# Optimization experiments

Measured on AMD Instinct MI355X. Metric: run time of the kernel, lower is better.

## Reference

```python
import jax, jax.numpy as jnp
import numpy as np

N_NODES = 50000
N_EDGES = 600000
D_IN = 128
HID = 128
N_SAGE = 2          # num_layers - 1
N_GRAPHS = 512
BN_EPS = 1e-5


def setup_inputs() -> dict:
    key = jax.random.key(0)
    ks = jax.random.split(key, 12)
    s = 1.0 / np.sqrt(HID)
    x = jax.random.normal(ks[0], (N_NODES, D_IN), dtype=jnp.float32)
    edge_index = jax.random.randint(ks[1], (2, N_EDGES), 0, N_NODES, dtype=jnp.int32)
    batch = jnp.sort(jax.random.randint(ks[2], (N_NODES,), 0, N_GRAPHS, dtype=jnp.int32))
    # GIN MLP: Linear(D_IN,HID) -> ReLU -> Linear(HID,HID)
    gin_w1 = jax.random.normal(ks[3], (D_IN, HID), dtype=jnp.float32) * s
    gin_b1 = jnp.zeros((HID,), jnp.float32)
    gin_w2 = jax.random.normal(ks[4], (HID, HID), dtype=jnp.float32) * s
    gin_b2 = jnp.zeros((HID,), jnp.float32)
    # SAGEConv layers: lin_l (neighbors, with bias), lin_r (root, no bias)
    sage_wl = jax.random.normal(ks[5], (N_SAGE, HID, HID), dtype=jnp.float32) * s
    sage_bl = jnp.zeros((N_SAGE, HID), jnp.float32)
    sage_wr = jax.random.normal(ks[6], (N_SAGE, HID, HID), dtype=jnp.float32) * s
    # BatchNorm per layer (3 layers)
    bn_gamma = jnp.ones((1 + N_SAGE, HID), jnp.float32)
    bn_beta = jnp.zeros((1 + N_SAGE, HID), jnp.float32)
    return {"x": x, "edge_index": edge_index, "batch": batch,
            "gin_w1": gin_w1, "gin_b1": gin_b1, "gin_w2": gin_w2, "gin_b2": gin_b2,
            "sage_wl": sage_wl, "sage_bl": sage_bl, "sage_wr": sage_wr,
            "bn_gamma": bn_gamma, "bn_beta": bn_beta}


def _batchnorm(h, gamma, beta):
    # training-mode BN over the node dimension (biased variance, as torch)
    mu = jnp.mean(h, axis=0)
    var = jnp.var(h, axis=0)
    return gamma * (h - mu) * jax.lax.rsqrt(var + BN_EPS) + beta


def reference(x, edge_index, batch, gin_w1, gin_b1, gin_w2, gin_b2,
              sage_wl, sage_bl, sage_wr, bn_gamma, bn_beta):
    n = x.shape[0]
    src, dst = edge_index[0], edge_index[1]

    # ---- Layer 0: GINConv (eps=0): mlp(x + sum_{j->i} x_j) ----
    agg = jax.ops.segment_sum(x[src], dst, num_segments=n)  # [N, D_IN]
    h = x + agg
    h = jax.nn.relu(h @ gin_w1 + gin_b1) @ gin_w2 + gin_b2
    h = jax.nn.relu(_batchnorm(h, bn_gamma[0], bn_beta[0]))
    # dropout is identity (eval mode)

    # degree for mean aggregation (shared across SAGE layers)
    deg = jax.ops.segment_sum(jnp.ones((src.shape[0],), h.dtype), dst, num_segments=n)
    inv_deg = (1.0 / jnp.maximum(deg, 1.0))[:, None]  # [N,1]

    # ---- SAGE layers: lin_l(mean_{j->i} h_j) + lin_r(h_i) ----
    for l in range(N_SAGE):
        neigh = jax.ops.segment_sum(h[src], dst, num_segments=n) * inv_deg
        h = neigh @ sage_wl[l] + sage_bl[l] + h @ sage_wr[l]
        h = jax.nn.relu(_batchnorm(h, bn_gamma[l + 1], bn_beta[l + 1]))

    # ---- global mean pool over batch ids ----
    sums = jax.ops.segment_sum(h, batch, num_segments=N_GRAPHS)  # [G, HID]
    counts = jax.ops.segment_sum(jnp.ones((n,), h.dtype), batch, num_segments=N_GRAPHS)
    return sums / jnp.maximum(counts, 1.0)[:, None]
```

## Files before the change

### kernel.cpp

```cpp
#include <hip/hip_runtime.h>

#define N_NODES 50000
#define N_EDGES 600000
#define HID 128
#define N_GRAPHS 512
#define BN_EPS 1e-5f
#define INV_N (1.0f / 50000.0f)

typedef __attribute__((ext_vector_type(8))) short bf16x8;
typedef __attribute__((ext_vector_type(4))) float f32x4;

__device__ __forceinline__ unsigned short f2b(float f) {
    unsigned u = __float_as_uint(f);
    return (unsigned short)((u + 0x7FFFu + ((u >> 16) & 1u)) >> 16);
}
__device__ __forceinline__ float b2f(unsigned short h) {
    return __uint_as_float(((unsigned)h) << 16);
}

#define CONVX_BLOCKS 6250
#define WCONV_BLOCKS 384
#define DEG_BLOCKS   2344
__global__ __launch_bounds__(256) void prep_kernel(
    const float* __restrict__ x, const float* __restrict__ gw1, const float* __restrict__ gw2,
    const float* __restrict__ swl, const float* __restrict__ swr, const int* __restrict__ dst,
    unsigned short* __restrict__ x16, unsigned short* __restrict__ wt, int* __restrict__ deg)
{
    int b = blockIdx.x;
    int t = threadIdx.x;
    if (b < CONVX_BLOCKS) {
        int gid = b * 256 + t;
        int i = gid >> 5, l = gid & 31;
        if (i >= N_NODES) return;
        int c0 = l * 4;
        float4 v = *(const float4*)(x + (size_t)i * 128 + c0);
        ushort4 o;
        o.x = f2b(v.x); o.y = f2b(v.y); o.z = f2b(v.z); o.w = f2b(v.w);
        *(ushort4*)(x16 + (size_t)i * 128 + c0) = o;
    } else if (b < CONVX_BLOCKS + WCONV_BLOCKS) {
        int gid = (b - CONVX_BLOCKS) * 256 + t;
        int m = gid >> 14;
        int e = gid & 16383;
        int k = e >> 7;
        int n = e & 127;
        const float* src = (m == 0) ? gw1 : (m == 1) ? gw2 : (m == 2) ? swl
                         : (m == 3) ? swr : (m == 4) ? (swl + 16384) : (swr + 16384);
        wt[m * 16384 + n * 128 + k] = f2b(src[k * 128 + n]);
    } else {
        int e = (b - CONVX_BLOCKS - WCONV_BLOCKS) * 256 + t;
        if (e < N_EDGES) atomicAdd(&deg[dst[e]], 1);
    }
}

#define ALLOC_BLOCKS 196
__global__ __launch_bounds__(256) void alloc_kernel(int* __restrict__ cursor,
                                                    int* __restrict__ row_beg,
                                                    float* __restrict__ inv_deg,
                                                    int* __restrict__ total,
                                                    const int* __restrict__ batch,
                                                    int* __restrict__ gstart) {
    if (blockIdx.x >= ALLOC_BLOCKS) {
        int g = (blockIdx.x - ALLOC_BLOCKS) * 256 + threadIdx.x;
        if (g > N_GRAPHS) return;
        int lo = 0, hi = N_NODES;
        while (lo < hi) {
            int mid = (lo + hi) >> 1;
            if (batch[mid] < g) lo = mid + 1; else hi = mid;
        }
        gstart[g] = lo;
        return;
    }
    __shared__ int tmp[256];
    __shared__ int base;
    int i = blockIdx.x * 256 + threadIdx.x;
    int d = (i < N_NODES) ? cursor[i] : 0;
    tmp[threadIdx.x] = d;
    __syncthreads();
#pragma unroll
    for (int off = 1; off < 256; off <<= 1) {
        int v = (threadIdx.x >= off) ? tmp[threadIdx.x - off] : 0;
        __syncthreads();
        tmp[threadIdx.x] += v;
        __syncthreads();
    }
    if (threadIdx.x == 255) base = atomicAdd(total, tmp[255]);
    __syncthreads();
    if (i < N_NODES) {
        int b = base + tmp[threadIdx.x] - d;
        row_beg[i] = b;
        cursor[i] = b;
        inv_deg[i] = 1.0f / fmaxf((float)d, 1.0f);
    }
}

__global__ void csr_fill_kernel(const int* __restrict__ src, const int* __restrict__ dst,
                                int* __restrict__ cursor, int* __restrict__ csr_src, int nE) {
    int e = blockIdx.x * blockDim.x + threadIdx.x;
    if (e < nE) {
        int pos = atomicAdd(&cursor[dst[e]], 1);
        csr_src[pos] = src[e];
    }
}

template<bool AFF, bool MEAN, bool HACT>
__global__ __launch_bounds__(256) void aggregate_kernel(
    const unsigned short* __restrict__ feat,
    const int* __restrict__ row_beg, const int* __restrict__ row_end,
    const int* __restrict__ csr_src,
    const float* __restrict__ stats, const float* __restrict__ gamma,
    const float* __restrict__ beta, const float* __restrict__ inv_deg,
    unsigned short* __restrict__ agg, unsigned short* __restrict__ hact, int n)
{
    int gid = blockIdx.x * blockDim.x + threadIdx.x;
    int node = gid >> 4;
    int lane = gid & 15;
    if (node >= n) return;
    int c0 = lane * 8;

    float cc[8], ss[8];
    if (AFF) {
#pragma unroll
        for (int j = 0; j < 8; j++) {
            int col = c0 + j;
            float mu = stats[col] * INV_N;
            float var = stats[128 + col] * INV_N - mu * mu;
            float rs = rsqrtf(var + BN_EPS);
            float c = gamma[col] * rs;
            cc[j] = c;
            ss[j] = beta[col] - mu * c;
        }
    }

    float a[8];
#pragma unroll
    for (int j = 0; j < 8; j++) a[j] = 0.f;

    int beg = row_beg[node];
    int end = row_end[node];
    int e = beg;
    for (; e + 3 < end; e += 4) {
        int s0 = csr_src[e];
        int s1 = csr_src[e + 1];
        int s2 = csr_src[e + 2];
        int s3 = csr_src[e + 3];
        bf16x8 v0 = *(const bf16x8*)(feat + (size_t)s0 * 128 + c0);
        bf16x8 v1 = *(const bf16x8*)(feat + (size_t)s1 * 128 + c0);
        bf16x8 v2 = *(const bf16x8*)(feat + (size_t)s2 * 128 + c0);
        bf16x8 v3 = *(const bf16x8*)(feat + (size_t)s3 * 128 + c0);
#pragma unroll
        for (int j = 0; j < 8; j++) {
            float t0 = b2f((unsigned short)v0[j]);
            float t1 = b2f((unsigned short)v1[j]);
            float t2 = b2f((unsigned short)v2[j]);
            float t3 = b2f((unsigned short)v3[j]);
            if (AFF) {
                t0 = fmaxf(t0 * cc[j] + ss[j], 0.f);
                t1 = fmaxf(t1 * cc[j] + ss[j], 0.f);
                t2 = fmaxf(t2 * cc[j] + ss[j], 0.f);
                t3 = fmaxf(t3 * cc[j] + ss[j], 0.f);
            }
            a[j] += (t0 + t1) + (t2 + t3);
        }
    }
    for (; e < end; e++) {
        int s0 = csr_src[e];
        bf16x8 v0 = *(const bf16x8*)(feat + (size_t)s0 * 128 + c0);
#pragma unroll
        for (int j = 0; j < 8; j++) {
            float t0 = b2f((unsigned short)v0[j]);
            if (AFF) t0 = fmaxf(t0 * cc[j] + ss[j], 0.f);
            a[j] += t0;
        }
    }

    if (MEAN) {
        float s = inv_deg[node];
#pragma unroll
        for (int j = 0; j < 8; j++) a[j] *= s;
    }
    bf16x8 o;
#pragma unroll
    for (int j = 0; j < 8; j++) o[j] = (short)f2b(a[j]);
    *(bf16x8*)(agg + (size_t)node * 128 + c0) = o;

    if (HACT) {
        bf16x8 v = *(const bf16x8*)(feat + (size_t)node * 128 + c0);
        bf16x8 h;
#pragma unroll
        for (int j = 0; j < 8; j++)
            h[j] = (short)f2b(fmaxf(b2f((unsigned short)v[j]) * cc[j] + ss[j], 0.f));
        *(bf16x8*)(hact + (size_t)node * 128 + c0) = h;
    }
}

__global__ __launch_bounds__(256, 2) void gemm_gin_kernel(
    const unsigned short* __restrict__ X, const unsigned short* __restrict__ AGG,
    const unsigned short* __restrict__ W1t, const unsigned short* __restrict__ W2t,
    const float* __restrict__ b1, const float* __restrict__ b2,
    float* __restrict__ stats, unsigned short* __restrict__ Cb,
    int M, int ntiles)
{
    __shared__ unsigned short t1[32][136];
    __shared__ float red[2][128];

    const int t = threadIdx.x;
    const int wave = t >> 6;
    const int lane = t & 63;
    const int colhalf = wave & 1;
    const int rowpair = wave >> 1;
    const int m16 = lane & 15;
    const int quad = lane >> 4;
    const int k0 = quad * 8;
    const int colbase = colhalf * 64;
    const int lrow = rowpair * 16 + m16;

    const bf16x8 zero8 = {0, 0, 0, 0, 0, 0, 0, 0};

    bf16x8 w1f[4][4], w2f[4][4];
#pragma unroll
    for (int ct = 0; ct < 4; ct++) {
        int col = colbase + ct * 16 + m16;
#pragma unroll
        for (int kc = 0; kc < 4; kc++) {
            w1f[ct][kc] = *(const bf16x8*)(W1t + (size_t)col * 128 + kc * 32 + k0);
            w2f[ct][kc] = *(const bf16x8*)(W2t + (size_t)col * 128 + kc * 32 + k0);
        }
    }
    f32x4 bs1[4], bs2[4];
#pragma unroll
    for (int ct = 0; ct < 4; ct++) {
        bs1[ct] = *(const f32x4*)(b1 + colbase + ct * 16 + quad * 4);
        bs2[ct] = *(const f32x4*)(b2 + colbase + ct * 16 + quad * 4);
    }

    float psum[4][4], psq[4][4];
#pragma unroll
    for (int ct = 0; ct < 4; ct++)
#pragma unroll
        for (int r = 0; r < 4; r++) { psum[ct][r] = 0.f; psq[ct][r] = 0.f; }

    for (int tile = blockIdx.x; tile < ntiles; tile += gridDim.x) {
        int arow = tile * 32 + rowpair * 16 + m16;
        bool aok = arow < M;

        bf16x8 a[4];
#pragma unroll
        for (int kc = 0; kc < 4; kc++) {
            if (aok) {
                bf16x8 vx = *(const bf16x8*)(X + (size_t)arow * 128 + kc * 32 + k0);
                bf16x8 vg = *(const bf16x8*)(AGG + (size_t)arow * 128 + kc * 32 + k0);
                bf16x8 r;
#pragma unroll
                for (int i = 0; i < 8; i++)
                    r[i] = (short)f2b(b2f((unsigned short)vx[i]) + b2f((unsigned short)vg[i]));
                a[kc] = r;
            } else {
                a[kc] = zero8;
            }
        }

        f32x4 acc[4];
#pragma unroll
        for (int ct = 0; ct < 4; ct++) acc[ct] = (f32x4){0.f, 0.f, 0.f, 0.f};
#pragma unroll
        for (int kc = 0; kc < 4; kc++)
#pragma unroll
            for (int ct = 0; ct < 4; ct++)
                acc[ct] = __builtin_amdgcn_mfma_f32_16x16x32_bf16(w1f[ct][kc], a[kc], acc[ct], 0, 0, 0);

        __syncthreads();
#pragma unroll
        for (int ct = 0; ct < 4; ct++) {
            f32x4 v = acc[ct] + bs1[ct];
            ushort4 o;
            o.x = f2b(fmaxf(v[0], 0.f));
            o.y = f2b(fmaxf(v[1], 0.f));
            o.z = f2b(fmaxf(v[2], 0.f));
            o.w = f2b(fmaxf(v[3], 0.f));
            *(ushort4*)&t1[lrow][colbase + ct * 16 + quad * 4] = o;
        }
        __syncthreads();

        bf16x8 ta[4];
#pragma unroll
        for (int kc = 0; kc < 4; kc++)
            ta[kc] = *(const bf16x8*)&t1[lrow][kc * 32 + k0];

        f32x4 acc2[4];
#pragma unroll
        for (int ct = 0; ct < 4; ct++) acc2[ct] = (f32x4){0.f, 0.f, 0.f, 0.f};
#pragma unroll
        for (int kc = 0; kc < 4; kc++)
#pragma unroll
            for (int ct = 0; ct < 4; ct++)
                acc2[ct] = __builtin_amdgcn_mfma_f32_16x16x32_bf16(w2f[ct][kc], ta[kc], acc2[ct], 0, 0, 0);

        int orow = arow;
        if (orow < M) {
#pragma unroll
            for (int ct = 0; ct < 4; ct++) {
                f32x4 v = acc2[ct] + bs2[ct];
                int col = colbase + ct * 16 + quad * 4;
#pragma unroll
                for (int r = 0; r < 4; r++) { psum[ct][r] += v[r]; psq[ct][r] += v[r] * v[r]; }
                ushort4 o;
                o.x = f2b(v[0]); o.y = f2b(v[1]); o.z = f2b(v[2]); o.w = f2b(v[3]);
                *(ushort4*)(Cb + (size_t)orow * 128 + col) = o;
            }
        }
    }

#pragma unroll
    for (int ct = 0; ct < 4; ct++)
#pragma unroll
        for (int r = 0; r < 4; r++) {
#pragma unroll
            for (int mask = 1; mask <= 8; mask <<= 1) {
                psum[ct][r] += __shfl_xor(psum[ct][r], mask, 64);
                psq[ct][r]  += __shfl_xor(psq[ct][r], mask, 64);
            }
        }
    __syncthreads();
    if (m16 == 0) {
#pragma unroll
        for (int ct = 0; ct < 4; ct++)
#pragma unroll
            for (int r = 0; r < 4; r++)
                red[rowpair][colbase + ct * 16 + quad * 4 + r] = psum[ct][r];
    }
    __syncthreads();
    if (t < 128) atomicAdd(&stats[t], red[0][t] + red[1][t]);
    __syncthreads();
    if (m16 == 0) {
#pragma unroll
        for (int ct = 0; ct < 4; ct++)
#pragma unroll
            for (int r = 0; r < 4; r++)
                red[rowpair][colbase + ct * 16 + quad * 4 + r] = psq[ct][r];
    }
    __syncthreads();
    if (t < 128) atomicAdd(&stats[128 + t], red[0][t] + red[1][t]);
}

__global__ __launch_bounds__(256) void gemm_dual_kernel(
    const unsigned short* __restrict__ A1, const unsigned short* __restrict__ A2,
    const unsigned short* __restrict__ W1t, const unsigned short* __restrict__ W2t,
    const float* __restrict__ bias, float* __restrict__ stats,
    unsigned short* __restrict__ Cb, int M, int ntiles)
{
    __shared__ float red[128];

    const int t = threadIdx.x;
    const int wave = t >> 6;
    const int lane = t & 63;
    const int m16 = lane & 15;
    const int quad = lane >> 4;
    const int k0 = quad * 8;
    const int colbase = wave * 32;

    const bf16x8 zero8 = {0, 0, 0, 0, 0, 0, 0, 0};

    bf16x8 w1f[2][4], w2f[2][4];
#pragma unroll
    for (int ct = 0; ct < 2; ct++) {
        int col = colbase + ct * 16 + m16;
#pragma unroll
        for (int kc = 0; kc < 4; kc++) {
            w1f[ct][kc] = *(const bf16x8*)(W1t + (size_t)col * 128 + kc * 32 + k0);
            w2f[ct][kc] = *(const bf16x8*)(W2t + (size_t)col * 128 + kc * 32 + k0);
        }
    }
    f32x4 bs[2];
#pragma unroll
    for (int ct = 0; ct < 2; ct++)
        bs[ct] = *(const f32x4*)(bias + colbase + ct * 16 + quad * 4);

    float psum[2][4], psq[2][4];
#pragma unroll
    for (int ct = 0; ct < 2; ct++)
#pragma unroll
        for (int r = 0; r < 4; r++) { psum[ct][r] = 0.f; psq[ct][r] = 0.f; }

    bf16x8 a1[4], a2[4], a1n[4], a2n[4];

    int tile = blockIdx.x;
    if (tile < ntiles) {
        int arow = tile * 16 + m16;
        bool aok = arow < M;
#pragma unroll
        for (int kc = 0; kc < 4; kc++) {
            a1[kc] = aok ? *(const bf16x8*)(A1 + (size_t)arow * 128 + kc * 32 + k0) : zero8;
            a2[kc] = aok ? *(const bf16x8*)(A2 + (size_t)arow * 128 + kc * 32 + k0) : zero8;
        }
    }

    for (; tile < ntiles; tile += gridDim.x) {
        int nt = tile + gridDim.x;
        if (nt < ntiles) {
            int arow = nt * 16 + m16;
            bool aok = arow < M;
#pragma unroll
            for (int kc = 0; kc < 4; kc++) {
                a1n[kc] = aok ? *(const bf16x8*)(A1 + (size_t)arow * 128 + kc * 32 + k0) : zero8;
                a2n[kc] = aok ? *(const bf16x8*)(A2 + (size_t)arow * 128 + kc * 32 + k0) : zero8;
            }
        }

        f32x4 acc[2];
        acc[0] = (f32x4){0.f, 0.f, 0.f, 0.f};
        acc[1] = (f32x4){0.f, 0.f, 0.f, 0.f};
#pragma unroll
        for (int kc = 0; kc < 4; kc++) {
#pragma unroll
            for (int ct = 0; ct < 2; ct++) {
                acc[ct] = __builtin_amdgcn_mfma_f32_16x16x32_bf16(w1f[ct][kc], a1[kc], acc[ct], 0, 0, 0);
                acc[ct] = __builtin_amdgcn_mfma_f32_16x16x32_bf16(w2f[ct][kc], a2[kc], acc[ct], 0, 0, 0);
            }
        }

        int orow = tile * 16 + m16;
        if (orow < M) {
#pragma unroll
            for (int ct = 0; ct < 2; ct++) {
                f32x4 v = acc[ct] + bs[ct];
                int col = colbase + ct * 16 + quad * 4;
#pragma unroll
                for (int r = 0; r < 4; r++) { psum[ct][r] += v[r]; psq[ct][r] += v[r] * v[r]; }
                ushort4 o;
                o.x = f2b(v[0]); o.y = f2b(v[1]); o.z = f2b(v[2]); o.w = f2b(v[3]);
                *(ushort4*)(Cb + (size_t)orow * 128 + col) = o;
            }
        }

        if (nt < ntiles) {
            a1[0] = a1n[0]; a1[1] = a1n[1]; a1[2] = a1n[2]; a1[3] = a1n[3];
            a2[0] = a2n[0]; a2[1] = a2n[1]; a2[2] = a2n[2]; a2[3] = a2n[3];
        }
    }

#pragma unroll
    for (int ct = 0; ct < 2; ct++)
#pragma unroll
        for (int r = 0; r < 4; r++) {
#pragma unroll
            for (int mask = 1; mask <= 8; mask <<= 1) {
                psum[ct][r] += __shfl_xor(psum[ct][r], mask, 64);
                psq[ct][r]  += __shfl_xor(psq[ct][r], mask, 64);
            }
        }
    if (m16 == 0) {
#pragma unroll
        for (int ct = 0; ct < 2; ct++)
#pragma unroll
            for (int r = 0; r < 4; r++)
                red[colbase + ct * 16 + quad * 4 + r] = psum[ct][r];
    }
    __syncthreads();
    if (t < 128) atomicAdd(&stats[t], red[t]);
    __syncthreads();
    if (m16 == 0) {
#pragma unroll
        for (int ct = 0; ct < 2; ct++)
#pragma unroll
            for (int r = 0; r < 4; r++)
                red[colbase + ct * 16 + quad * 4 + r] = psq[ct][r];
    }
    __syncthreads();
    if (t < 128) atomicAdd(&stats[128 + t], red[t]);
}

__global__ __launch_bounds__(128) void pool_mean_kernel(const unsigned short* __restrict__ h,
                                                        const int* __restrict__ gstart,
                                                        const float* __restrict__ stats,
                                                        const float* __restrict__ gamma,
                                                        const float* __restrict__ beta,
                                                        float* __restrict__ out) {
    int g = blockIdx.x;
    int col = threadIdx.x;
    float mu = stats[col] * INV_N;
    float var = stats[128 + col] * INV_N - mu * mu;
    float rs = rsqrtf(var + BN_EPS);
    float c = gamma[col] * rs;
    float b = beta[col] - mu * c;
    int beg = gstart[g];
    int end = gstart[g + 1];
    float s = 0.f;
    int i = beg;
    for (; i + 1 < end; i += 2) {
        float v0 = b2f(h[(size_t)i * 128 + col]);
        float v1 = b2f(h[(size_t)(i + 1) * 128 + col]);
        s += fmaxf(v0 * c + b, 0.f) + fmaxf(v1 * c + b, 0.f);
    }
    if (i < end)
        s += fmaxf(b2f(h[(size_t)i * 128 + col]) * c + b, 0.f);
    float cnt = fmaxf((float)(end - beg), 1.0f);
    out[(size_t)g * 128 + col] = s / cnt;
}

extern "C" void kernel_launch(void* const* d_in, const int* in_sizes, int n_in,
                              void* d_out, int out_size, void* d_ws, size_t ws_size,
                              hipStream_t stream) {
    const float* x    = (const float*)d_in[0];
    const int*   ei   = (const int*)d_in[1];
    const int*   src  = ei;
    const int*   dst  = ei + N_EDGES;
    const int*   batch = (const int*)d_in[2];
    const float* gw1  = (const float*)d_in[3];
    const float* gb1  = (const float*)d_in[4];
    const float* gw2  = (const float*)d_in[5];
    const float* gb2  = (const float*)d_in[6];
    const float* swl  = (const float*)d_in[7];
    const float* sbl  = (const float*)d_in[8];
    const float* swr  = (const float*)d_in[9];
    const float* bng  = (const float*)d_in[10];
    const float* bnb  = (const float*)d_in[11];
    float* out = (float*)d_out;

    float* ws = (float*)d_ws;
    unsigned short* x16    = (unsigned short*)(ws + 0);
    unsigned short* agg16  = (unsigned short*)(ws + 3200000);
    unsigned short* hact16 = (unsigned short*)(ws + 6400000);
    unsigned short* hpre16 = (unsigned short*)(ws + 9600000);
    unsigned short* wt     = (unsigned short*)(ws + 12800000);
    float*          inv_deg= ws + 12850000;
    int*            row_beg= (int*)(ws + 12900000);
    int*            cursor = (int*)(ws + 12950000);
    int*            total  = cursor + 50000;
    float*          stats  = (float*)(cursor + 50001);
    int*            csr_src= (int*)(ws + 13100000);
    int*            gstart = (int*)(ws + 13700000);

    const int aggr_blocks = (N_NODES * 16 + 255) / 256;
    const int ntiles32 = (N_NODES + 31) / 32;
    const int ntiles16 = (N_NODES + 15) / 16;
    const int ggrid = 512;

    hipMemsetAsync(cursor, 0, (50001 + 768) * sizeof(int), stream);

    prep_kernel<<<CONVX_BLOCKS + WCONV_BLOCKS + DEG_BLOCKS, 256, 0, stream>>>(
        x, gw1, gw2, swl, swr, dst, x16, wt, cursor);

    alloc_kernel<<<ALLOC_BLOCKS + 3, 256, 0, stream>>>(cursor, row_beg, inv_deg, total, batch, gstart);
    csr_fill_kernel<<<(N_EDGES + 255) / 256, 256, 0, stream>>>(src, dst, cursor, csr_src, N_EDGES);

    aggregate_kernel<false, false, false><<<aggr_blocks, 256, 0, stream>>>(
        x16, row_beg, cursor, csr_src, nullptr, nullptr, nullptr, nullptr, agg16, nullptr, N_NODES);
    gemm_gin_kernel<<<ggrid, 256, 0, stream>>>(
        x16, agg16, wt + 0 * 16384, wt + 1 * 16384, gb1, gb2, stats + 0, hpre16, N_NODES, ntiles32);

    aggregate_kernel<true, true, true><<<aggr_blocks, 256, 0, stream>>>(
        hpre16, row_beg, cursor, csr_src, stats + 0, bng + 0 * HID, bnb + 0 * HID, inv_deg,
        agg16, hact16, N_NODES);
    gemm_dual_kernel<<<ggrid, 256, 0, stream>>>(
        agg16, hact16, wt + 2 * 16384, wt + 3 * 16384, sbl + 0 * HID, stats + 256, hpre16, N_NODES, ntiles16);

    aggregate_kernel<true, true, true><<<aggr_blocks, 256, 0, stream>>>(
        hpre16, row_beg, cursor, csr_src, stats + 256, bng + 1 * HID, bnb + 1 * HID, inv_deg,
        agg16, hact16, N_NODES);
    gemm_dual_kernel<<<ggrid, 256, 0, stream>>>(
        agg16, hact16, wt + 4 * 16384, wt + 5 * 16384, sbl + 1 * HID, stats + 512, hpre16, N_NODES, ntiles16);

    pool_mean_kernel<<<N_GRAPHS, 128, 0, stream>>>(
        hpre16, gstart, stats + 512, bng + 2 * HID, bnb + 2 * HID, out);
}
```

Measured before the change: 362.7 us.

## Fuse neighbor aggregation with per-layer GEMMs into single kernels per layer

Merges each layer's gather/aggregate kernel with its following MFMA GEMM. A 16-row tile is aggregated into shared memory and multiplied in the same block. This removes the intermediate agg/hact buffers and their HBM write-read round trips, plus three kernel launches. The cost is that gather latency and MFMA work are now serialized within each block, with extra barriers per tile and weights held in registers, which could reduce occupancy. Ping-pong hpre buffers avoid read/write aliasing.

```diff
diff --git a/kernel.cpp b/kernel.cpp
--- a/kernel.cpp
+++ b/kernel.cpp
@@ -102,255 +102,23 @@
     }
 }
 
-template<bool AFF, bool MEAN, bool HACT>
-__global__ __launch_bounds__(256) void aggregate_kernel(
-    const unsigned short* __restrict__ feat,
+__global__ __launch_bounds__(256) void gin_fused_kernel(
+    const unsigned short* __restrict__ x16,
     const int* __restrict__ row_beg, const int* __restrict__ row_end,
     const int* __restrict__ csr_src,
-    const float* __restrict__ stats, const float* __restrict__ gamma,
-    const float* __restrict__ beta, const float* __restrict__ inv_deg,
-    unsigned short* __restrict__ agg, unsigned short* __restrict__ hact, int n)
-{
-    int gid = blockIdx.x * blockDim.x + threadIdx.x;
-    int node = gid >> 4;
-    int lane = gid & 15;
-    if (node >= n) return;
-    int c0 = lane * 8;
-
-    float cc[8], ss[8];
-    if (AFF) {
-#pragma unroll
-        for (int j = 0; j < 8; j++) {
-            int col = c0 + j;
-            float mu = stats[col] * INV_N;
-            float var = stats[128 + col] * INV_N - mu * mu;
-            float rs = rsqrtf(var + BN_EPS);
-            float c = gamma[col] * rs;
-            cc[j] = c;
-            ss[j] = beta[col] - mu * c;
-        }
-    }
-
-    float a[8];
-#pragma unroll
-    for (int j = 0; j < 8; j++) a[j] = 0.f;
-
-    int beg = row_beg[node];
-    int end = row_end[node];
-    int e = beg;
-    for (; e + 3 < end; e += 4) {
-        int s0 = csr_src[e];
-        int s1 = csr_src[e + 1];
-        int s2 = csr_src[e + 2];
-        int s3 = csr_src[e + 3];
-        bf16x8 v0 = *(const bf16x8*)(feat + (size_t)s0 * 128 + c0);
-        bf16x8 v1 = *(const bf16x8*)(feat + (size_t)s1 * 128 + c0);
-        bf16x8 v2 = *(const bf16x8*)(feat + (size_t)s2 * 128 + c0);
-        bf16x8 v3 = *(const bf16x8*)(feat + (size_t)s3 * 128 + c0);
-#pragma unroll
-        for (int j = 0; j < 8; j++) {
-            float t0 = b2f((unsigned short)v0[j]);
-            float t1 = b2f((unsigned short)v1[j]);
-            float t2 = b2f((unsigned short)v2[j]);
-            float t3 = b2f((unsigned short)v3[j]);
-            if (AFF) {
-                t0 = fmaxf(t0 * cc[j] + ss[j], 0.f);
-                t1 = fmaxf(t1 * cc[j] + ss[j], 0.f);
-                t2 = fmaxf(t2 * cc[j] + ss[j], 0.f);
-                t3 = fmaxf(t3 * cc[j] + ss[j], 0.f);
-            }
-            a[j] += (t0 + t1) + (t2 + t3);
-        }
-    }
-    for (; e < end; e++) {
-        int s0 = csr_src[e];
-        bf16x8 v0 = *(const bf16x8*)(feat + (size_t)s0 * 128 + c0);
-#pragma unroll
-        for (int j = 0; j < 8; j++) {
-            float t0 = b2f((unsigned short)v0[j]);
-            if (AFF) t0 = fmaxf(t0 * cc[j] + ss[j], 0.f);
-            a[j] += t0;
-        }
-    }
-
-    if (MEAN) {
-        float s = inv_deg[node];
-#pragma unroll
-        for (int j = 0; j < 8; j++) a[j] *= s;
-    }
-    bf16x8 o;
-#pragma unroll
-    for (int j = 0; j < 8; j++) o[j] = (short)f2b(a[j]);
-    *(bf16x8*)(agg + (size_t)node * 128 + c0) = o;
-
-    if (HACT) {
-        bf16x8 v = *(const bf16x8*)(feat + (size_t)node * 128 + c0);
-        bf16x8 h;
-#pragma unroll
-        for (int j = 0; j < 8; j++)
-            h[j] = (short)f2b(fmaxf(b2f((unsigned short)v[j]) * cc[j] + ss[j], 0.f));
-        *(bf16x8*)(hact + (size_t)node * 128 + c0) = h;
-    }
-}
-
-__global__ __launch_bounds__(256, 2) void gemm_gin_kernel(
-    const unsigned short* __restrict__ X, const unsigned short* __restrict__ AGG,
     const unsigned short* __restrict__ W1t, const unsigned short* __restrict__ W2t,
     const float* __restrict__ b1, const float* __restrict__ b2,
-    float* __restrict__ stats, unsigned short* __restrict__ Cb,
-    int M, int ntiles)
+    float* __restrict__ stats, unsigned short* __restrict__ Cb, int ntiles)
 {
-    __shared__ unsigned short t1[32][136];
-    __shared__ float red[2][128];
+    __shared__ unsigned short As[16][136];
+    __shared__ unsigned short T1[16][136];
+    __shared__ float red[128];
 
     const int t = threadIdx.x;
-    const int wave = t >> 6;
-    const int lane = t & 63;
-    const int colhalf = wave & 1;
-    const int rowpair = wave >> 1;
-    const int m16 = lane & 15;
-    const int quad = lane >> 4;
-    const int k0 = quad * 8;
-    const int colbase = colhalf * 64;
-    const int lrow = rowpair * 16 + m16;
-
-    const bf16x8 zero8 = {0, 0, 0, 0, 0, 0, 0, 0};
-
-    bf16x8 w1f[4][4], w2f[4][4];
-#pragma unroll
-    for (int ct = 0; ct < 4; ct++) {
-        int col = colbase + ct * 16 + m16;
-#pragma unroll
-        for (int kc = 0; kc < 4; kc++) {
-            w1f[ct][kc] = *(const bf16x8*)(W1t + (size_t)col * 128 + kc * 32 + k0);
-            w2f[ct][kc] = *(const bf16x8*)(W2t + (size_t)col * 128 + kc * 32 + k0);
-        }
-    }
-    f32x4 bs1[4], bs2[4];
-#pragma unroll
-    for (int ct = 0; ct < 4; ct++) {
-        bs1[ct] = *(const f32x4*)(b1 + colbase + ct * 16 + quad * 4);
-        bs2[ct] = *(const f32x4*)(b2 + colbase + ct * 16 + quad * 4);
-    }
-
-    float psum[4][4], psq[4][4];
-#pragma unroll
-    for (int ct = 0; ct < 4; ct++)
-#pragma unroll
-        for (int r = 0; r < 4; r++) { psum[ct][r] = 0.f; psq[ct][r] = 0.f; }
-
-    for (int tile = blockIdx.x; tile < ntiles; tile += gridDim.x) {
-        int arow = tile * 32 + rowpair * 16 + m16;
-        bool aok = arow < M;
-
-        bf16x8 a[4];
-#pragma unroll
-        for (int kc = 0; kc < 4; kc++) {
-            if (aok) {
-                bf16x8 vx = *(const bf16x8*)(X + (size_t)arow * 128 + kc * 32 + k0);
-                bf16x8 vg = *(const bf16x8*)(AGG + (size_t)arow * 128 + kc * 32 + k0);
-                bf16x8 r;
-#pragma unroll
-                for (int i = 0; i < 8; i++)
-                    r[i] = (short)f2b(b2f((unsigned short)vx[i]) + b2f((unsigned short)vg[i]));
-                a[kc] = r;
-            } else {
-                a[kc] = zero8;
-            }
-        }
-
-        f32x4 acc[4];
-#pragma unroll
-        for (int ct = 0; ct < 4; ct++) acc[ct] = (f32x4){0.f, 0.f, 0.f, 0.f};
-#pragma unroll
-        for (int kc = 0; kc < 4; kc++)
-#pragma unroll
-            for (int ct = 0; ct < 4; ct++)
-                acc[ct] = __builtin_amdgcn_mfma_f32_16x16x32_bf16(w1f[ct][kc], a[kc], acc[ct], 0, 0, 0);
-
-        __syncthreads();
-#pragma unroll
-        for (int ct = 0; ct < 4; ct++) {
-            f32x4 v = acc[ct] + bs1[ct];
-            ushort4 o;
-            o.x = f2b(fmaxf(v[0], 0.f));
-            o.y = f2b(fmaxf(v[1], 0.f));
-            o.z = f2b(fmaxf(v[2], 0.f));
-            o.w = f2b(fmaxf(v[3], 0.f));
-            *(ushort4*)&t1[lrow][colbase + ct * 16 + quad * 4] = o;
-        }
-        __syncthreads();
-
-        bf16x8 ta[4];
-#pragma unroll
-        for (int kc = 0; kc < 4; kc++)
-            ta[kc] = *(const bf16x8*)&t1[lrow][kc * 32 + k0];
-
-        f32x4 acc2[4];
-#pragma unroll
-        for (int ct = 0; ct < 4; ct++) acc2[ct] = (f32x4){0.f, 0.f, 0.f, 0.f};
-#pragma unroll
-        for (int kc = 0; kc < 4; kc++)
-#pragma unroll
-            for (int ct = 0; ct < 4; ct++)
-                acc2[ct] = __builtin_amdgcn_mfma_f32_16x16x32_bf16(w2f[ct][kc], ta[kc], acc2[ct], 0, 0, 0);
-
-        int orow = arow;
-        if (orow < M) {
-#pragma unroll
-            for (int ct = 0; ct < 4; ct++) {
-                f32x4 v = acc2[ct] + bs2[ct];
-                int col = colbase + ct * 16 + quad * 4;
-#pragma unroll
-                for (int r = 0; r < 4; r++) { psum[ct][r] += v[r]; psq[ct][r] += v[r] * v[r]; }
-                ushort4 o;
-                o.x = f2b(v[0]); o.y = f2b(v[1]); o.z = f2b(v[2]); o.w = f2b(v[3]);
-                *(ushort4*)(Cb + (size_t)orow * 128 + col) = o;
-            }
-        }
-    }
-
-#pragma unroll
-    for (int ct = 0; ct < 4; ct++)
-#pragma unroll
-        for (int r = 0; r < 4; r++) {
-#pragma unroll
-            for (int mask = 1; mask <= 8; mask <<= 1) {
-                psum[ct][r] += __shfl_xor(psum[ct][r], mask, 64);
-                psq[ct][r]  += __shfl_xor(psq[ct][r], mask, 64);
-            }
-        }
-    __syncthreads();
-    if (m16 == 0) {
-#pragma unroll
-        for (int ct = 0; ct < 4; ct++)
-#pragma unroll
-            for (int r = 0; r < 4; r++)
-                red[rowpair][colbase + ct * 16 + quad * 4 + r] = psum[ct][r];
-    }
-    __syncthreads();
-    if (t < 128) atomicAdd(&stats[t], red[0][t] + red[1][t]);
-    __syncthreads();
-    if (m16 == 0) {
-#pragma unroll
-        for (int ct = 0; ct < 4; ct++)
-#pragma unroll
-            for (int r = 0; r < 4; r++)
-                red[rowpair][colbase + ct * 16 + quad * 4 + r] = psq[ct][r];
-    }
-    __syncthreads();
-    if (t < 128) atomicAdd(&stats[128 + t], red[0][t] + red[1][t]);
-}
-
-__global__ __launch_bounds__(256) void gemm_dual_kernel(
-    const unsigned short* __restrict__ A1, const unsigned short* __restrict__ A2,
-    const unsigned short* __restrict__ W1t, const unsigned short* __restrict__ W2t,
-    const float* __restrict__ bias, float* __restrict__ stats,
-    unsigned short* __restrict__ Cb, int M, int ntiles)
-{
-    __shared__ float red[128];
-
-    const int t = threadIdx.x;
+    const int srow = t >> 4;
+    const int sub = t & 15;
+    const int sc0 = sub * 8;
+
     const int wave = t >> 6;
     const int lane = t & 63;
     const int m16 = lane & 15;
@@ -358,8 +126,6 @@
     const int k0 = quad * 8;
     const int colbase = wave * 32;
 
-    const bf16x8 zero8 = {0, 0, 0, 0, 0, 0, 0, 0};
-
     bf16x8 w1f[2][4], w2f[2][4];
 #pragma unroll
     for (int ct = 0; ct < 2; ct++) {
@@ -370,71 +136,100 @@
             w2f[ct][kc] = *(const bf16x8*)(W2t + (size_t)col * 128 + kc * 32 + k0);
         }
     }
-    f32x4 bs[2];
+    f32x4 bs1[2], bs2[2];
+#pragma unroll
+    for (int ct = 0; ct < 2; ct++) {
+        bs1[ct] = *(const f32x4*)(b1 + colbase + ct * 16 + quad * 4);
+        bs2[ct] = *(const f32x4*)(b2 + colbase + ct * 16 + quad * 4);
+    }
+
+    float psum[2][4], psq[2][4];
 #pragma unroll
     for (int ct = 0; ct < 2; ct++)
-        bs[ct] = *(const f32x4*)(bias + colbase + ct * 16 + quad * 4);
-
-    float psum[2][4], psq[2][4];
-#pragma unroll
-    for (int ct = 0; ct < 2; ct++)
 #pragma unroll
         for (int r = 0; r < 4; r++) { psum[ct][r] = 0.f; psq[ct][r] = 0.f; }
 
-    bf16x8 a1[4], a2[4], a1n[4], a2n[4];
-
-    int tile = blockIdx.x;
-    if (tile < ntiles) {
-        int arow = tile * 16 + m16;
-        bool aok = arow < M;
-#pragma unroll
-        for (int kc = 0; kc < 4; kc++) {
-            a1[kc] = aok ? *(const bf16x8*)(A1 + (size_t)arow * 128 + kc * 32 + k0) : zero8;
-            a2[kc] = aok ? *(const bf16x8*)(A2 + (size_t)arow * 128 + kc * 32 + k0) : zero8;
-        }
-    }
-
-    for (; tile < ntiles; tile += gridDim.x) {
-        int nt = tile + gridDim.x;
-        if (nt < ntiles) {
-            int arow = nt * 16 + m16;
-            bool aok = arow < M;
-#pragma unroll
-            for (int kc = 0; kc < 4; kc++) {
-                a1n[kc] = aok ? *(const bf16x8*)(A1 + (size_t)arow * 128 + kc * 32 + k0) : zero8;
-                a2n[kc] = aok ? *(const bf16x8*)(A2 + (size_t)arow * 128 + kc * 32 + k0) : zero8;
-            }
-        }
-
-        f32x4 acc[2];
-        acc[0] = (f32x4){0.f, 0.f, 0.f, 0.f};
-        acc[1] = (f32x4){0.f, 0.f, 0.f, 0.f};
-#pragma unroll
-        for (int kc = 0; kc < 4; kc++) {
-#pragma unroll
-            for (int ct = 0; ct < 2; ct++) {
-                acc[ct] = __builtin_amdgcn_mfma_f32_16x16x32_bf16(w1f[ct][kc], a1[kc], acc[ct], 0, 0, 0);
-                acc[ct] = __builtin_amdgcn_mfma_f32_16x16x32_bf16(w2f[ct][kc], a2[kc], acc[ct], 0, 0, 0);
-            }
-        }
+    for (int tile = blockIdx.x; tile < ntiles; tile += gridDim.x) {
+        int grow = tile * 16 + srow;
+        int beg = row_beg[grow];
+        int end = row_end[grow];
+        bf16x8 own = *(const bf16x8*)(x16 + (size_t)grow * 128 + sc0);
+        float acc[8];
+#pragma unroll
+        for (int j = 0; j < 8; j++) acc[j] = b2f((unsigned short)own[j]);
+
+        int e = beg;
+        for (; e + 3 < end; e += 4) {
+            int s0 = csr_src[e], s1 = csr_src[e + 1], s2 = csr_src[e + 2], s3 = csr_src[e + 3];
+            bf16x8 v0 = *(const bf16x8*)(x16 + (size_t)s0 * 128 + sc0);
+            bf16x8 v1 = *(const bf16x8*)(x16 + (size_t)s1 * 128 + sc0);
+            bf16x8 v2 = *(const bf16x8*)(x16 + (size_t)s2 * 128 + sc0);
+            bf16x8 v3 = *(const bf16x8*)(x16 + (size_t)s3 * 128 + sc0);
+#pragma unroll
+            for (int j = 0; j < 8; j++)
+                acc[j] += (b2f((unsigned short)v0[j]) + b2f((unsigned short)v1[j]))
+                        + (b2f((unsigned short)v2[j]) + b2f((unsigned short)v3[j]));
+        }
+        for (; e < end; e++) {
+            int s0 = csr_src[e];
+            bf16x8 v0 = *(const bf16x8*)(x16 + (size_t)s0 * 128 + sc0);
+#pragma unroll
+            for (int j = 0; j < 8; j++) acc[j] += b2f((unsigned short)v0[j]);
+        }
+
+        __syncthreads();
+        bf16x8 o;
+#pragma unroll
+        for (int j = 0; j < 8; j++) o[j] = (short)f2b(acc[j]);
+        *(bf16x8*)&As[srow][sc0] = o;
+        __syncthreads();
+
+        bf16x8 a[4];
+#pragma unroll
+        for (int kc = 0; kc < 4; kc++) a[kc] = *(const bf16x8*)&As[m16][kc * 32 + k0];
+        f32x4 acc1[2];
+        acc1[0] = (f32x4){0.f, 0.f, 0.f, 0.f};
+        acc1[1] = (f32x4){0.f, 0.f, 0.f, 0.f};
+#pragma unroll
+        for (int kc = 0; kc < 4; kc++)
+#pragma unroll
+            for (int ct = 0; ct < 2; ct++)
+                acc1[ct] = __builtin_amdgcn_mfma_f32_16x16x32_bf16(w1f[ct][kc], a[kc], acc1[ct], 0, 0, 0);
+
+#pragma unroll
+        for (int ct = 0; ct < 2; ct++) {
+            f32x4 v = acc1[ct] + bs1[ct];
+            ushort4 u;
+            u.x = f2b(fmaxf(v[0], 0.f));
+            u.y = f2b(fmaxf(v[1], 0.f));
+            u.z = f2b(fmaxf(v[2], 0.f));
+            u.w = f2b(fmaxf(v[3], 0.f));
+            *(ushort4*)&T1[m16][colbase + ct * 16 + quad * 4] = u;
+        }
+        __syncthreads();
+
+        bf16x8 ta[4];
+#pragma unroll
+        for (int kc = 0; kc < 4; kc++) ta[kc] = *(const bf16x8*)&T1[m16][kc * 32 + k0];
+        f32x4 acc2[2];
+        acc2[0] = (f32x4){0.f, 0.f, 0.f, 0.f};
+        acc2[1] = (f32x4){0.f, 0.f, 0.f, 0.f};
+#pragma unroll
+        for (int kc = 0; kc < 4; kc++)
+#pragma unroll
+            for (int ct = 0; ct < 2; ct++)
+                acc2[ct] = __builtin_amdgcn_mfma_f32_16x16x32_bf16(w2f[ct][kc], ta[kc], acc2[ct], 0, 0, 0);
 
         int orow = tile * 16 + m16;
-        if (orow < M) {
-#pragma unroll
-            for (int ct = 0; ct < 2; ct++) {
-                f32x4 v = acc[ct] + bs[ct];
-                int col = colbase + ct * 16 + quad * 4;
-#pragma unroll
-                for (int r = 0; r < 4; r++) { psum[ct][r] += v[r]; psq[ct][r] += v[r] * v[r]; }
-                ushort4 o;
-                o.x = f2b(v[0]); o.y = f2b(v[1]); o.z = f2b(v[2]); o.w = f2b(v[3]);
-                *(ushort4*)(Cb + (size_t)orow * 128 + col) = o;
-            }
-        }
-
-        if (nt < ntiles) {
-            a1[0] = a1n[0]; a1[1] = a1n[1]; a1[2] = a1n[2]; a1[3] = a1n[3];
-            a2[0] = a2n[0]; a2[1] = a2n[1]; a2[2] = a2n[2]; a2[3] = a2n[3];
+#pragma unroll
+        for (int ct = 0; ct < 2; ct++) {
+            f32x4 v = acc2[ct] + bs2[ct];
+            int col = colbase + ct * 16 + quad * 4;
+#pragma unroll
+            for (int r = 0; r < 4; r++) { psum[ct][r] += v[r]; psq[ct][r] += v[r] * v[r]; }
+            ushort4 u;
+            u.x = f2b(v[0]); u.y = f2b(v[1]); u.z = f2b(v[2]); u.w = f2b(v[3]);
+            *(ushort4*)(Cb + (size_t)orow * 128 + col) = u;
         }
     }
 
@@ -448,6 +243,7 @@
                 psq[ct][r]  += __shfl_xor(psq[ct][r], mask, 64);
             }
         }
+    __syncthreads();
     if (m16 == 0) {
 #pragma unroll
         for (int ct = 0; ct < 2; ct++)
@@ -467,6 +263,174 @@
     }
     __syncthreads();
     if (t < 128) atomicAdd(&stats[128 + t], red[t]);
+}
+
+__global__ __launch_bounds__(256) void sage_fused_kernel(
+    const unsigned short* __restrict__ feat,
+    const int* __restrict__ row_beg, const int* __restrict__ row_end,
+    const int* __restrict__ csr_src,
+    const float* __restrict__ stats_in, const float* __restrict__ gamma,
+    const float* __restrict__ beta, const float* __restrict__ inv_deg,
+    const unsigned short* __restrict__ W1t, const unsigned short* __restrict__ W2t,
+    const float* __restrict__ bias,
+    float* __restrict__ stats_out, unsigned short* __restrict__ Cb, int ntiles)
+{
+    __shared__ unsigned short As1[16][136];
+    __shared__ unsigned short As2[16][136];
+    __shared__ float red[128];
+
+    const int t = threadIdx.x;
+    const int srow = t >> 4;
+    const int sub = t & 15;
+    const int sc0 = sub * 8;
+
+    const int wave = t >> 6;
+    const int lane = t & 63;
+    const int m16 = lane & 15;
+    const int quad = lane >> 4;
+    const int k0 = quad * 8;
+    const int colbase = wave * 32;
+
+    float cc[8], ss[8];
+#pragma unroll
+    for (int j = 0; j < 8; j++) {
+        int col = sc0 + j;
+        float mu = stats_in[col] * INV_N;
+        float var = stats_in[128 + col] * INV_N - mu * mu;
+        float rs = rsqrtf(var + BN_EPS);
+        float c = gamma[col] * rs;
+        cc[j] = c;
+        ss[j] = beta[col] - mu * c;
+    }
+
+    bf16x8 w1f[2][4], w2f[2][4];
+#pragma unroll
+    for (int ct = 0; ct < 2; ct++) {
+        int col = colbase + ct * 16 + m16;
+#pragma unroll
+        for (int kc = 0; kc < 4; kc++) {
+            w1f[ct][kc] = *(const bf16x8*)(W1t + (size_t)col * 128 + kc * 32 + k0);
+            w2f[ct][kc] = *(const bf16x8*)(W2t + (size_t)col * 128 + kc * 32 + k0);
+        }
+    }
+    f32x4 bs[2];
+#pragma unroll
+    for (int ct = 0; ct < 2; ct++)
+        bs[ct] = *(const f32x4*)(bias + colbase + ct * 16 + quad * 4);
+
+    float psum[2][4], psq[2][4];
+#pragma unroll
+    for (int ct = 0; ct < 2; ct++)
+#pragma unroll
+        for (int r = 0; r < 4; r++) { psum[ct][r] = 0.f; psq[ct][r] = 0.f; }
+
+    for (int tile = blockIdx.x; tile < ntiles; tile += gridDim.x) {
+        int grow = tile * 16 + srow;
+        int beg = row_beg[grow];
+        int end = row_end[grow];
+        float idg = inv_deg[grow];
+        bf16x8 own = *(const bf16x8*)(feat + (size_t)grow * 128 + sc0);
+
+        float acc[8];
+#pragma unroll
+        for (int j = 0; j < 8; j++) acc[j] = 0.f;
+
+        int e = beg;
+        for (; e + 3 < end; e += 4) {
+            int s0 = csr_src[e], s1 = csr_src[e + 1], s2 = csr_src[e + 2], s3 = csr_src[e + 3];
+            bf16x8 v0 = *(const bf16x8*)(feat + (size_t)s0 * 128 + sc0);
+            bf16x8 v1 = *(const bf16x8*)(feat + (size_t)s1 * 128 + sc0);
+            bf16x8 v2 = *(const bf16x8*)(feat + (size_t)s2 * 128 + sc0);
+            bf16x8 v3 = *(const bf16x8*)(feat + (size_t)s3 * 128 + sc0);
+#pragma unroll
+            for (int j = 0; j < 8; j++) {
+                float t0 = fmaxf(b2f((unsigned short)v0[j]) * cc[j] + ss[j], 0.f);
+                float t1 = fmaxf(b2f((unsigned short)v1[j]) * cc[j] + ss[j], 0.f);
+                float t2 = fmaxf(b2f((unsigned short)v2[j]) * cc[j] + ss[j], 0.f);
+                float t3 = fmaxf(b2f((unsigned short)v3[j]) * cc[j] + ss[j], 0.f);
+                acc[j] += (t0 + t1) + (t2 + t3);
+            }
+        }
+        for (; e < end; e++) {
+            int s0 = csr_src[e];
+            bf16x8 v0 = *(const bf16x8*)(feat + (size_t)s0 * 128 + sc0);
+#pragma unroll
+            for (int j = 0; j < 8; j++)
+                acc[j] += fmaxf(b2f((unsigned short)v0[j]) * cc[j] + ss[j], 0.f);
+        }
+
+        __syncthreads();
+        bf16x8 o1, o2;
+#pragma unroll
+        for (int j = 0; j < 8; j++) {
+            o1[j] = (short)f2b(acc[j] * idg);
+            o2[j] = (short)f2b(fmaxf(b2f((unsigned short)own[j]) * cc[j] + ss[j], 0.f));
+        }
+        *(bf16x8*)&As1[srow][sc0] = o1;
+        *(bf16x8*)&As2[srow][sc0] = o2;
+        __syncthreads();
+
+        bf16x8 a1[4], a2[4];
+#pragma unroll
+        for (int kc = 0; kc < 4; kc++) {
+            a1[kc] = *(const bf16x8*)&As1[m16][kc * 32 + k0];
+            a2[kc] = *(const bf16x8*)&As2[m16][kc * 32 + k0];
+        }
+        f32x4 acc2[2];
+        acc2[0] = (f32x4){0.f, 0.f, 0.f, 0.f};
+        acc2[1] = (f32x4){0.f, 0.f, 0.f, 0.f};
+#pragma unroll
+        for (int kc = 0; kc < 4; kc++) {
+#pragma unroll
+            for (int ct = 0; ct < 2; ct++) {
+                acc2[ct] = __builtin_amdgcn_mfma_f32_16x16x32_bf16(w1f[ct][kc], a1[kc], acc2[ct], 0, 0, 0);
+                acc2[ct] = __builtin_amdgcn_mfma_f32_16x16x32_bf16(w2f[ct][kc], a2[kc], acc2[ct], 0, 0, 0);
+            }
+        }
+
+        int orow = tile * 16 + m16;
+#pragma unroll
+        for (int ct = 0; ct < 2; ct++) {
+            f32x4 v = acc2[ct] + bs[ct];
+            int col = colbase + ct * 16 + quad * 4;
+#pragma unroll
+            for (int r = 0; r < 4; r++) { psum[ct][r] += v[r]; psq[ct][r] += v[r] * v[r]; }
+            ushort4 u;
+            u.x = f2b(v[0]); u.y = f2b(v[1]); u.z = f2b(v[2]); u.w = f2b(v[3]);
+            *(ushort4*)(Cb + (size_t)orow * 128 + col) = u;
+        }
+    }
+
+#pragma unroll
+    for (int ct = 0; ct < 2; ct++)
+#pragma unroll
+        for (int r = 0; r < 4; r++) {
+#pragma unroll
+            for (int mask = 1; mask <= 8; mask <<= 1) {
+                psum[ct][r] += __shfl_xor(psum[ct][r], mask, 64);
+                psq[ct][r]  += __shfl_xor(psq[ct][r], mask, 64);
+            }
+        }
+    __syncthreads();
+    if (m16 == 0) {
+#pragma unroll
+        for (int ct = 0; ct < 2; ct++)
+#pragma unroll
+            for (int r = 0; r < 4; r++)
+                red[colbase + ct * 16 + quad * 4 + r] = psum[ct][r];
+    }
+    __syncthreads();
+    if (t < 128) atomicAdd(&stats_out[t], red[t]);
+    __syncthreads();
+    if (m16 == 0) {
+#pragma unroll
+        for (int ct = 0; ct < 2; ct++)
+#pragma unroll
+            for (int r = 0; r < 4; r++)
+                red[colbase + ct * 16 + quad * 4 + r] = psq[ct][r];
+    }
+    __syncthreads();
+    if (t < 128) atomicAdd(&stats_out[128 + t], red[t]);
 }
 
 __global__ __launch_bounds__(128) void pool_mean_kernel(const unsigned short* __restrict__ h,
@@ -518,22 +482,19 @@
 
     float* ws = (float*)d_ws;
     unsigned short* x16    = (unsigned short*)(ws + 0);
-    unsigned short* agg16  = (unsigned short*)(ws + 3200000);
-    unsigned short* hact16 = (unsigned short*)(ws + 6400000);
-    unsigned short* hpre16 = (unsigned short*)(ws + 9600000);
-    unsigned short* wt     = (unsigned short*)(ws + 12800000);
-    float*          inv_deg= ws + 12850000;
-    int*            row_beg= (int*)(ws + 12900000);
-    int*            cursor = (int*)(ws + 12950000);
+    unsigned short* hpreA  = (unsigned short*)(ws + 3200000);
+    unsigned short* hpreB  = (unsigned short*)(ws + 6400000);
+    unsigned short* wt     = (unsigned short*)(ws + 9600000);
+    float*          inv_deg= ws + 9650000;
+    int*            row_beg= (int*)(ws + 9700000);
+    int*            cursor = (int*)(ws + 9750000);
     int*            total  = cursor + 50000;
     float*          stats  = (float*)(cursor + 50001);
-    int*            csr_src= (int*)(ws + 13100000);
-    int*            gstart = (int*)(ws + 13700000);
-
-    const int aggr_blocks = (N_NODES * 16 + 255) / 256;
-    const int ntiles32 = (N_NODES + 31) / 32;
-    const int ntiles16 = (N_NODES + 15) / 16;
-    const int ggrid = 512;
+    int*            csr_src= (int*)(ws + 9900000);
+    int*            gstart = (int*)(ws + 10500000);
+
+    const int ntiles16 = N_NODES / 16;
+    const int fgrid = 1024;
 
     hipMemsetAsync(cursor, 0, (50001 + 768) * sizeof(int), stream);
 
@@ -543,23 +504,18 @@
     alloc_kernel<<<ALLOC_BLOCKS + 3, 256, 0, stream>>>(cursor, row_beg, inv_deg, total, batch, gstart);
     csr_fill_kernel<<<(N_EDGES + 255) / 256, 256, 0, stream>>>(src, dst, cursor, csr_src, N_EDGES);
 
-    aggregate_kernel<false, false, false><<<aggr_blocks, 256, 0, stream>>>(
-        x16, row_beg, cursor, csr_src, nullptr, nullptr, nullptr, nullptr, agg16, nullptr, N_NODES);
-    gemm_gin_kernel<<<ggrid, 256, 0, stream>>>(
-        x16, agg16, wt + 0 * 16384, wt + 1 * 16384, gb1, gb2, stats + 0, hpre16, N_NODES, ntiles32);
-
-    aggregate_kernel<true, true, true><<<aggr_blocks, 256, 0, stream>>>(
-        hpre16, row_beg, cursor, csr_src, stats + 0, bng + 0 * HID, bnb + 0 * HID, inv_deg,
-        agg16, hact16, N_NODES);
-    gemm_dual_kernel<<<ggrid, 256, 0, stream>>>(
-        agg16, hact16, wt + 2 * 16384, wt + 3 * 16384, sbl + 0 * HID, stats + 256, hpre16, N_NODES, ntiles16);
-
-    aggregate_kernel<true, true, true><<<aggr_blocks, 256, 0, stream>>>(
-        hpre16, row_beg, cursor, csr_src, stats + 256, bng + 1 * HID, bnb + 1 * HID, inv_deg,
-        agg16, hact16, N_NODES);
-    gemm_dual_kernel<<<ggrid, 256, 0, stream>>>(
-        agg16, hact16, wt + 4 * 16384, wt + 5 * 16384, sbl + 1 * HID, stats + 512, hpre16, N_NODES, ntiles16);
+    gin_fused_kernel<<<fgrid, 256, 0, stream>>>(
+        x16, row_beg, cursor, csr_src, wt + 0 * 16384, wt + 1 * 16384,
+        gb1, gb2, stats + 0, hpreA, ntiles16);
+
+    sage_fused_kernel<<<fgrid, 256, 0, stream>>>(
+        hpreA, row_beg, cursor, csr_src, stats + 0, bng + 0 * HID, bnb + 0 * HID, inv_deg,
+        wt + 2 * 16384, wt + 3 * 16384, sbl + 0 * HID, stats + 256, hpreB, ntiles16);
+
+    sage_fused_kernel<<<fgrid, 256, 0, stream>>>(
+        hpreB, row_beg, cursor, csr_src, stats + 256, bng + 1 * HID, bnb + 1 * HID, inv_deg,
+        wt + 4 * 16384, wt + 5 * 16384, sbl + 1 * HID, stats + 512, hpreA, ntiles16);
 
     pool_mean_kernel<<<N_GRAPHS, 128, 0, stream>>>(
-        hpre16, gstart, stats + 512, bng + 2 * HID, bnb + 2 * HID, out);
-}
+        hpreA, gstart, stats + 512, bng + 2 * HID, bnb + 2 * HID, out);
+}
```

Result: slower. 403.9 us (+11.3%).
